# Optimization experiments

Hardware: AMD Instinct MI355X
Metric: run time of the kernel (lower is better)

## Reference

```python
import jax, jax.numpy as jnp
import numpy as np

B = 4194304  # batch
H = 32       # hidden width of TinyMLP


def _xavier(key, fan_in, fan_out, gain=0.5):
    lim = gain * np.sqrt(6.0 / (fan_in + fan_out))
    return jax.random.uniform(key, (fan_in, fan_out), jnp.float32, -lim, lim)


def setup_inputs() -> dict:
    key = jax.random.key(0)
    ks = jax.random.split(key, 7)
    return {
        "x1": jax.random.normal(ks[0], (B,), jnp.float32),
        "x2": jax.random.normal(ks[1], (B,), jnp.float32),
        "y1": jax.random.normal(ks[2], (B,), jnp.float32),
        "y2": jax.random.normal(ks[3], (B,), jnp.float32),
        "W1": _xavier(ks[4], 2, H),
        "b1": jnp.zeros((H,), jnp.float32),
        "W2": _xavier(ks[5], H, H),
        "b2": jnp.zeros((H,), jnp.float32),
        "W3": _xavier(ks[6], H, 1),
        "b3": jnp.zeros((1,), jnp.float32),
    }


def reference(x1, x2, y1, y2, W1, b1, W2, b2, W3, b3):
    # Y: [B, 2]
    Y = jnp.stack([y1, y2], axis=1)

    def F_sum(Yv):
        h1 = jax.nn.sigmoid(Yv @ W1 + b1)   # [B, H]
        h2 = jax.nn.sigmoid(h1 @ W2 + b2)   # [B, H]
        return jnp.sum(h2 @ W3 + b3)        # scalar sum of F values

    dF_dY = jax.grad(F_sum)(Y)              # [B, 2], analytic input-gradient

    x1_out = x1 + dF_dY[:, 0]
    x2_out = x2 + dF_dY[:, 1]
    # Stack the 4 output streams as columns: (x1', x2', y1, y2)
    return jnp.stack([x1_out, x2_out, y1, y2], axis=1)
```

## Files before the change

### kernel.cpp

```cpp
#include <hip/hip_runtime.h>


#define H 32
#define NLOG2E (-1.4426950408889634f)

typedef __attribute__((ext_vector_type(8))) short bf16x8;
typedef __attribute__((ext_vector_type(16))) float f32x16;
typedef __attribute__((ext_vector_type(2))) float f32x2;
typedef __attribute__((ext_vector_type(2))) __bf16 bfx2;

#define MFMA32 __builtin_amdgcn_mfma_f32_32x32x16_bf16

__device__ __forceinline__ int cvt_pk_bf16(float a, float b) {
    f32x2 f; f[0] = a; f[1] = b;
    bfx2 r = __builtin_convertvector(f, bfx2);
    return __builtin_bit_cast(int, r);
}
__device__ __forceinline__ float pklo(int p) {
    unsigned u = (unsigned)p << 16; return __builtin_bit_cast(float, u);
}
__device__ __forceinline__ float pkhi(int p) {
    unsigned u = (unsigned)p & 0xFFFF0000u; return __builtin_bit_cast(float, u);
}

__device__ __forceinline__ void plane32_swap(int &d, int &s) {
    asm volatile("v_permlane32_swap_b32 %0, %1" : "+v"(d), "+v"(s));
}

__global__ __launch_bounds__(256, 6) void tinymlp_mfma_kernel(
    const float* __restrict__ x1, const float* __restrict__ x2,
    const float* __restrict__ y1, const float* __restrict__ y2,
    const float* __restrict__ W1, const float* __restrict__ b1,
    const float* __restrict__ W2, const float* __restrict__ b2,
    const float* __restrict__ W3,
    float4* __restrict__ out, int ntiles)
{
    const int tid  = threadIdx.x;
    const int lane = tid & 63;
    const int n    = lane & 31;
    const int q5   = lane >> 5;

    union U4 { int i[4]; bf16x8 v; };
    U4 A_z1, A_z2a, A_z2b, A_dh1a, A_dh1b, A_dya, A_dyb;

    #pragma unroll
    for (int t = 0; t < 4; ++t) {
        const int j0 = 8 * q5 + 2 * t;
        const int j1 = j0 + 1;
        A_z2a.i[t] = cvt_pk_bf16(NLOG2E * W2[j0 * H + n],        NLOG2E * W2[j1 * H + n]);
        A_z2b.i[t] = cvt_pk_bf16(NLOG2E * W2[(16 + j0) * H + n], NLOG2E * W2[(16 + j1) * H + n]);
        A_dh1a.i[t] = cvt_pk_bf16(W2[n * H + j0] * W3[j0],           W2[n * H + j1] * W3[j1]);
        A_dh1b.i[t] = cvt_pk_bf16(W2[n * H + 16 + j0] * W3[16 + j0], W2[n * H + 16 + j1] * W3[16 + j1]);
        A_dya.i[t] = (n < 2) ? cvt_pk_bf16(W1[n * H + j0],      W1[n * H + j1])      : 0;
        A_dyb.i[t] = (n < 2) ? cvt_pk_bf16(W1[n * H + 16 + j0], W1[n * H + 16 + j1]) : 0;
    }

    A_z1.i[0] = A_z1.i[1] = A_z1.i[2] = A_z1.i[3] = 0;
    if (q5 == 0) {
        const float wa = NLOG2E * W1[n];
        const float wb = NLOG2E * W1[H + n];
        const float bv = NLOG2E * b1[n];
        const int hi  = cvt_pk_bf16(wa, wb);
        const int lo  = cvt_pk_bf16(wa - pklo(hi), wb - pkhi(hi));
        const int bh  = cvt_pk_bf16(bv, 0.f);
        const int bhl = cvt_pk_bf16(bv, bv - pklo(bh));
        A_z1.i[0] = hi; A_z1.i[1] = lo; A_z1.i[2] = hi; A_z1.i[3] = bhl;
    }

    f32x16 b2C;
    #pragma unroll
    for (int t = 0; t < 4; ++t) {
        const float4 bt = *(const float4*)&b2[8 * t + 4 * q5];
        b2C[4 * t + 0] = NLOG2E * bt.x; b2C[4 * t + 1] = NLOG2E * bt.y;
        b2C[4 * t + 2] = NLOG2E * bt.z; b2C[4 * t + 3] = NLOG2E * bt.w;
    }

    f32x16 zf16;
    #pragma unroll
    for (int r = 0; r < 16; ++r) zf16[r] = 0.f;

    const int gwave  = (blockIdx.x * blockDim.x + tid) >> 6;
    const int nwaves = (gridDim.x * blockDim.x) >> 6;
    unsigned idx = (unsigned)gwave * 32 + (unsigned)n;
    const unsigned step = (unsigned)nwaves * 32;

    for (int tt = gwave; tt < ntiles; tt += nwaves) {
        float y1v = 0.f, y2v = 0.f, xv1 = 0.f, xv2 = 0.f;
        if (lane < 32) {
            y1v = y1[idx]; y2v = y2[idx];
            xv1 = x1[idx]; xv2 = x2[idx];
        }

        U4 uY;
        const int pkHI = cvt_pk_bf16(y1v, y2v);
        const int pkLO = cvt_pk_bf16(y1v - pklo(pkHI), y2v - pkhi(pkHI));
        uY.i[0] = pkHI; uY.i[1] = pkHI; uY.i[2] = pkLO;
        uY.i[3] = 0x3F803F80;

        const f32x16 acc = MFMA32(A_z1.v, uY.v, zf16, 0, 0, 0);

        int P[8];
        #pragma unroll
        for (int h = 0; h < 2; ++h) {
            const int o = 8 * h;
            f32x2 A, Bv, Cv, Dv;
            A[0]  = __builtin_amdgcn_exp2f(acc[o + 0]);
            A[1]  = __builtin_amdgcn_exp2f(acc[o + 1]);
            Bv[0] = __builtin_amdgcn_exp2f(acc[o + 2]);
            Bv[1] = __builtin_amdgcn_exp2f(acc[o + 3]);
            Cv[0] = __builtin_amdgcn_exp2f(acc[o + 4]);
            Cv[1] = __builtin_amdgcn_exp2f(acc[o + 5]);
            Dv[0] = __builtin_amdgcn_exp2f(acc[o + 6]);
            Dv[1] = __builtin_amdgcn_exp2f(acc[o + 7]);
            A += 1.0f; Bv += 1.0f; Cv += 1.0f; Dv += 1.0f;
            const f32x2 M1 = A * Bv, M2 = Cv * Dv, M = M1 * M2;
            const float r = __builtin_amdgcn_rcpf(M[0] * M[1]);
            f32x2 R; R[0] = r * M[1]; R[1] = r * M[0];
            const f32x2 N1 = R * M2, N2 = R * M1;
            const f32x2 S0 = Bv * N1, S1 = A * N1, S2 = Dv * N2, S3 = Cv * N2;
            P[4 * h + 0] = cvt_pk_bf16(S0[0], S0[1]);
            P[4 * h + 1] = cvt_pk_bf16(S1[0], S1[1]);
            P[4 * h + 2] = cvt_pk_bf16(S2[0], S2[1]);
            P[4 * h + 3] = cvt_pk_bf16(S3[0], S3[1]);
        }

        U4 B1f, B2f;
        {
            int a0 = P[0], a2 = P[2]; plane32_swap(a0, a2);
            int a1 = P[1], a3 = P[3]; plane32_swap(a1, a3);
            B1f.i[0] = a0; B1f.i[1] = a1; B1f.i[2] = a2; B1f.i[3] = a3;
            int b0 = P[4], b2i = P[6]; plane32_swap(b0, b2i);
            int b1i = P[5], b3 = P[7]; plane32_swap(b1i, b3);
            B2f.i[0] = b0; B2f.i[1] = b1i; B2f.i[2] = b2i; B2f.i[3] = b3;
        }

        f32x16 zz = MFMA32(A_z2a.v, B1f.v, b2C, 0, 0, 0);
        zz = MFMA32(A_z2b.v, B2f.v, zz, 0, 0, 0);

        U4 D1f, D2f;
        #pragma unroll
        for (int h = 0; h < 2; ++h) {
            const int o = 8 * h;
            f32x2 A, Bv, Cv, Dv;
            A[0]  = __builtin_amdgcn_exp2f(zz[o + 0]);
            A[1]  = __builtin_amdgcn_exp2f(zz[o + 1]);
            Bv[0] = __builtin_amdgcn_exp2f(zz[o + 2]);
            Bv[1] = __builtin_amdgcn_exp2f(zz[o + 3]);
            Cv[0] = __builtin_amdgcn_exp2f(zz[o + 4]);
            Cv[1] = __builtin_amdgcn_exp2f(zz[o + 5]);
            Dv[0] = __builtin_amdgcn_exp2f(zz[o + 6]);
            Dv[1] = __builtin_amdgcn_exp2f(zz[o + 7]);
            A += 1.0f; Bv += 1.0f; Cv += 1.0f; Dv += 1.0f;
            const f32x2 M1 = A * Bv, M2 = Cv * Dv, M = M1 * M2;
            const float r = __builtin_amdgcn_rcpf(M[0] * M[1]);
            f32x2 R; R[0] = r * M[1]; R[1] = r * M[0];
            const f32x2 N1 = R * M2, N2 = R * M1;
            f32x2 S0 = Bv * N1, S1 = A * N1, S2 = Dv * N2, S3 = Cv * N2;
            S0 = __builtin_elementwise_fma(-S0, S0, S0);
            S1 = __builtin_elementwise_fma(-S1, S1, S1);
            S2 = __builtin_elementwise_fma(-S2, S2, S2);
            S3 = __builtin_elementwise_fma(-S3, S3, S3);
            U4& Df = h ? D2f : D1f;
            Df.i[0] = cvt_pk_bf16(S0[0], S0[1]);
            Df.i[1] = cvt_pk_bf16(S1[0], S1[1]);
            Df.i[2] = cvt_pk_bf16(S2[0], S2[1]);
            Df.i[3] = cvt_pk_bf16(S3[0], S3[1]);
        }
        plane32_swap(D1f.i[0], D1f.i[2]);
        plane32_swap(D1f.i[1], D1f.i[3]);
        plane32_swap(D2f.i[0], D2f.i[2]);
        plane32_swap(D2f.i[1], D2f.i[3]);

        f32x16 dh = MFMA32(A_dh1a.v, D1f.v, zf16, 0, 0, 0);
        dh = MFMA32(A_dh1b.v, D2f.v, dh, 0, 0, 0);

        U4 E1f, E2f;
        #pragma unroll
        for (int t = 0; t < 4; ++t) {
            U4& Ef = (t & 2) ? E2f : E1f;
            const int sl = 2 * (t & 1);
            f32x2 sv, gg;
            sv[0] = pklo(P[2 * t]); sv[1] = pkhi(P[2 * t]);
            sv = __builtin_elementwise_fma(-sv, sv, sv);
            gg[0] = dh[4 * t]; gg[1] = dh[4 * t + 1]; gg *= sv;
            Ef.i[sl] = cvt_pk_bf16(gg[0], gg[1]);
            sv[0] = pklo(P[2 * t + 1]); sv[1] = pkhi(P[2 * t + 1]);
            sv = __builtin_elementwise_fma(-sv, sv, sv);
            gg[0] = dh[4 * t + 2]; gg[1] = dh[4 * t + 3]; gg *= sv;
            Ef.i[sl + 1] = cvt_pk_bf16(gg[0], gg[1]);
        }
        plane32_swap(E1f.i[0], E1f.i[2]);
        plane32_swap(E1f.i[1], E1f.i[3]);
        plane32_swap(E2f.i[0], E2f.i[2]);
        plane32_swap(E2f.i[1], E2f.i[3]);

        f32x16 ay = MFMA32(A_dya.v, E1f.v, zf16, 0, 0, 0);
        ay = MFMA32(A_dyb.v, E2f.v, ay, 0, 0, 0);

        if (lane < 32) {
            float4 o;
            o.x = xv1 + ay[0];
            o.y = xv2 + ay[1];
            o.z = y1v;
            o.w = y2v;
            out[idx] = o;
        }

        idx += step;
    }
}

extern "C" void kernel_launch(void* const* d_in, const int* in_sizes, int n_in,
                              void* d_out, int out_size, void* d_ws, size_t ws_size,
                              hipStream_t stream) {
    const float* x1 = (const float*)d_in[0];
    const float* x2 = (const float*)d_in[1];
    const float* y1 = (const float*)d_in[2];
    const float* y2 = (const float*)d_in[3];
    const float* W1 = (const float*)d_in[4];
    const float* b1 = (const float*)d_in[5];
    const float* W2 = (const float*)d_in[6];
    const float* b2 = (const float*)d_in[7];
    const float* W3 = (const float*)d_in[8];

    const int n = in_sizes[0];
    const int ntiles = n / 32;
    const int block = 256;
    const int grid = 1536;
    tinymlp_mfma_kernel<<<grid, block, 0, stream>>>(
        x1, x2, y1, y2, W1, b1, W2, b2, W3, (float4*)d_out, ntiles);
}
```

Measured before the change: 208.6 us.

## Process two 32-row tiles per wave iteration to interleave MFMA chains

Each loop iteration now handles two independent tiles, A and B, with their MFMA and sigmoid stages interleaved. This is meant to hide MFMA latency and the serial dependency stalls within a single wave through instruction-level parallelism. To pay for the extra register use, the occupancy target in launch_bounds drops from 6 to 4 and the grid shrinks from 1536 to 1024 blocks. The code assumes ntiles is even, because odd leftover tiles would be dropped.

```diff
diff --git a/kernel.cpp b/kernel.cpp
--- a/kernel.cpp
+++ b/kernel.cpp
@@ -27,7 +27,7 @@
     asm volatile("v_permlane32_swap_b32 %0, %1" : "+v"(d), "+v"(s));
 }
 
-__global__ __launch_bounds__(256, 6) void tinymlp_mfma_kernel(
+__global__ __launch_bounds__(256, 4) void tinymlp_mfma_kernel(
     const float* __restrict__ x1, const float* __restrict__ x2,
     const float* __restrict__ y1, const float* __restrict__ y2,
     const float* __restrict__ W1, const float* __restrict__ b1,
@@ -79,39 +79,24 @@
     #pragma unroll
     for (int r = 0; r < 16; ++r) zf16[r] = 0.f;
 
-    const int gwave  = (blockIdx.x * blockDim.x + tid) >> 6;
-    const int nwaves = (gridDim.x * blockDim.x) >> 6;
-    unsigned idx = (unsigned)gwave * 32 + (unsigned)n;
-    const unsigned step = (unsigned)nwaves * 32;
-
-    for (int tt = gwave; tt < ntiles; tt += nwaves) {
-        float y1v = 0.f, y2v = 0.f, xv1 = 0.f, xv2 = 0.f;
-        if (lane < 32) {
-            y1v = y1[idx]; y2v = y2[idx];
-            xv1 = x1[idx]; xv2 = x2[idx];
-        }
-
-        U4 uY;
-        const int pkHI = cvt_pk_bf16(y1v, y2v);
-        const int pkLO = cvt_pk_bf16(y1v - pklo(pkHI), y2v - pkhi(pkHI));
-        uY.i[0] = pkHI; uY.i[1] = pkHI; uY.i[2] = pkLO;
-        uY.i[3] = 0x3F803F80;
-
-        const f32x16 acc = MFMA32(A_z1.v, uY.v, zf16, 0, 0, 0);
-
-        int P[8];
+    auto mkY = [&](float a, float b, U4& u) {
+        const int hi = cvt_pk_bf16(a, b);
+        const int lo = cvt_pk_bf16(a - pklo(hi), b - pkhi(hi));
+        u.i[0] = hi; u.i[1] = hi; u.i[2] = lo; u.i[3] = 0x3F803F80;
+    };
+    auto sig8 = [&](const f32x16& z, int* P) {
         #pragma unroll
         for (int h = 0; h < 2; ++h) {
             const int o = 8 * h;
             f32x2 A, Bv, Cv, Dv;
-            A[0]  = __builtin_amdgcn_exp2f(acc[o + 0]);
-            A[1]  = __builtin_amdgcn_exp2f(acc[o + 1]);
-            Bv[0] = __builtin_amdgcn_exp2f(acc[o + 2]);
-            Bv[1] = __builtin_amdgcn_exp2f(acc[o + 3]);
-            Cv[0] = __builtin_amdgcn_exp2f(acc[o + 4]);
-            Cv[1] = __builtin_amdgcn_exp2f(acc[o + 5]);
-            Dv[0] = __builtin_amdgcn_exp2f(acc[o + 6]);
-            Dv[1] = __builtin_amdgcn_exp2f(acc[o + 7]);
+            A[0]  = __builtin_amdgcn_exp2f(z[o + 0]);
+            A[1]  = __builtin_amdgcn_exp2f(z[o + 1]);
+            Bv[0] = __builtin_amdgcn_exp2f(z[o + 2]);
+            Bv[1] = __builtin_amdgcn_exp2f(z[o + 3]);
+            Cv[0] = __builtin_amdgcn_exp2f(z[o + 4]);
+            Cv[1] = __builtin_amdgcn_exp2f(z[o + 5]);
+            Dv[0] = __builtin_amdgcn_exp2f(z[o + 6]);
+            Dv[1] = __builtin_amdgcn_exp2f(z[o + 7]);
             A += 1.0f; Bv += 1.0f; Cv += 1.0f; Dv += 1.0f;
             const f32x2 M1 = A * Bv, M2 = Cv * Dv, M = M1 * M2;
             const float r = __builtin_amdgcn_rcpf(M[0] * M[1]);
@@ -123,21 +108,16 @@
             P[4 * h + 2] = cvt_pk_bf16(S2[0], S2[1]);
             P[4 * h + 3] = cvt_pk_bf16(S3[0], S3[1]);
         }
-
-        U4 B1f, B2f;
-        {
-            int a0 = P[0], a2 = P[2]; plane32_swap(a0, a2);
-            int a1 = P[1], a3 = P[3]; plane32_swap(a1, a3);
-            B1f.i[0] = a0; B1f.i[1] = a1; B1f.i[2] = a2; B1f.i[3] = a3;
-            int b0 = P[4], b2i = P[6]; plane32_swap(b0, b2i);
-            int b1i = P[5], b3 = P[7]; plane32_swap(b1i, b3);
-            B2f.i[0] = b0; B2f.i[1] = b1i; B2f.i[2] = b2i; B2f.i[3] = b3;
-        }
-
-        f32x16 zz = MFMA32(A_z2a.v, B1f.v, b2C, 0, 0, 0);
-        zz = MFMA32(A_z2b.v, B2f.v, zz, 0, 0, 0);
-
-        U4 D1f, D2f;
+    };
+    auto pivP = [&](const int* P, U4& F1, U4& F2) {
+        int a0 = P[0], a2 = P[2]; plane32_swap(a0, a2);
+        int a1 = P[1], a3 = P[3]; plane32_swap(a1, a3);
+        F1.i[0] = a0; F1.i[1] = a1; F1.i[2] = a2; F1.i[3] = a3;
+        int b0 = P[4], b2i = P[6]; plane32_swap(b0, b2i);
+        int b1i = P[5], b3 = P[7]; plane32_swap(b1i, b3);
+        F2.i[0] = b0; F2.i[1] = b1i; F2.i[2] = b2i; F2.i[3] = b3;
+    };
+    auto dz2f = [&](const f32x16& zz, U4& D1, U4& D2) {
         #pragma unroll
         for (int h = 0; h < 2; ++h) {
             const int o = 8 * h;
@@ -160,24 +140,21 @@
             S1 = __builtin_elementwise_fma(-S1, S1, S1);
             S2 = __builtin_elementwise_fma(-S2, S2, S2);
             S3 = __builtin_elementwise_fma(-S3, S3, S3);
-            U4& Df = h ? D2f : D1f;
+            U4& Df = h ? D2 : D1;
             Df.i[0] = cvt_pk_bf16(S0[0], S0[1]);
             Df.i[1] = cvt_pk_bf16(S1[0], S1[1]);
             Df.i[2] = cvt_pk_bf16(S2[0], S2[1]);
             Df.i[3] = cvt_pk_bf16(S3[0], S3[1]);
         }
-        plane32_swap(D1f.i[0], D1f.i[2]);
-        plane32_swap(D1f.i[1], D1f.i[3]);
-        plane32_swap(D2f.i[0], D2f.i[2]);
-        plane32_swap(D2f.i[1], D2f.i[3]);
-
-        f32x16 dh = MFMA32(A_dh1a.v, D1f.v, zf16, 0, 0, 0);
-        dh = MFMA32(A_dh1b.v, D2f.v, dh, 0, 0, 0);
-
-        U4 E1f, E2f;
+        plane32_swap(D1.i[0], D1.i[2]);
+        plane32_swap(D1.i[1], D1.i[3]);
+        plane32_swap(D2.i[0], D2.i[2]);
+        plane32_swap(D2.i[1], D2.i[3]);
+    };
+    auto dz1f = [&](const f32x16& dh, const int* P, U4& E1, U4& E2) {
         #pragma unroll
         for (int t = 0; t < 4; ++t) {
-            U4& Ef = (t & 2) ? E2f : E1f;
+            U4& Ef = (t & 2) ? E2 : E1;
             const int sl = 2 * (t & 1);
             f32x2 sv, gg;
             sv[0] = pklo(P[2 * t]); sv[1] = pkhi(P[2 * t]);
@@ -189,21 +166,78 @@
             gg[0] = dh[4 * t + 2]; gg[1] = dh[4 * t + 3]; gg *= sv;
             Ef.i[sl + 1] = cvt_pk_bf16(gg[0], gg[1]);
         }
-        plane32_swap(E1f.i[0], E1f.i[2]);
-        plane32_swap(E1f.i[1], E1f.i[3]);
-        plane32_swap(E2f.i[0], E2f.i[2]);
-        plane32_swap(E2f.i[1], E2f.i[3]);
-
-        f32x16 ay = MFMA32(A_dya.v, E1f.v, zf16, 0, 0, 0);
-        ay = MFMA32(A_dyb.v, E2f.v, ay, 0, 0, 0);
-
+        plane32_swap(E1.i[0], E1.i[2]);
+        plane32_swap(E1.i[1], E1.i[3]);
+        plane32_swap(E2.i[0], E2.i[2]);
+        plane32_swap(E2.i[1], E2.i[3]);
+    };
+
+    const int gpair  = (blockIdx.x * blockDim.x + tid) >> 6;
+    const int nwaves = (gridDim.x * blockDim.x) >> 6;
+    const int npairs = ntiles >> 1;
+    unsigned idx = (unsigned)gpair * 64 + (unsigned)n;
+    const unsigned step = (unsigned)nwaves * 64;
+
+    for (int pp = gpair; pp < npairs; pp += nwaves) {
+        float yA1 = 0.f, yA2 = 0.f, xA1 = 0.f, xA2 = 0.f;
+        float yB1 = 0.f, yB2 = 0.f, xB1 = 0.f, xB2 = 0.f;
         if (lane < 32) {
-            float4 o;
-            o.x = xv1 + ay[0];
-            o.y = xv2 + ay[1];
-            o.z = y1v;
-            o.w = y2v;
-            out[idx] = o;
+            yA1 = y1[idx];      yA2 = y2[idx];
+            yB1 = y1[idx + 32]; yB2 = y2[idx + 32];
+            xA1 = x1[idx];      xA2 = x2[idx];
+            xB1 = x1[idx + 32]; xB2 = x2[idx + 32];
+        }
+
+        U4 uYA, uYB;
+        mkY(yA1, yA2, uYA);
+        mkY(yB1, yB2, uYB);
+        const f32x16 accA = MFMA32(A_z1.v, uYA.v, zf16, 0, 0, 0);
+        const f32x16 accB = MFMA32(A_z1.v, uYB.v, zf16, 0, 0, 0);
+
+        int PA[8], PB[8];
+        sig8(accA, PA);
+        sig8(accB, PB);
+
+        U4 B1A, B2A, B1B, B2B;
+        pivP(PA, B1A, B2A);
+        pivP(PB, B1B, B2B);
+
+        f32x16 zzA = MFMA32(A_z2a.v, B1A.v, b2C, 0, 0, 0);
+        f32x16 zzB = MFMA32(A_z2a.v, B1B.v, b2C, 0, 0, 0);
+        zzA = MFMA32(A_z2b.v, B2A.v, zzA, 0, 0, 0);
+        zzB = MFMA32(A_z2b.v, B2B.v, zzB, 0, 0, 0);
+
+        U4 D1A, D2A, D1B, D2B;
+        dz2f(zzA, D1A, D2A);
+        dz2f(zzB, D1B, D2B);
+
+        f32x16 dhA = MFMA32(A_dh1a.v, D1A.v, zf16, 0, 0, 0);
+        f32x16 dhB = MFMA32(A_dh1a.v, D1B.v, zf16, 0, 0, 0);
+        dhA = MFMA32(A_dh1b.v, D2A.v, dhA, 0, 0, 0);
+        dhB = MFMA32(A_dh1b.v, D2B.v, dhB, 0, 0, 0);
+
+        U4 E1A, E2A, E1B, E2B;
+        dz1f(dhA, PA, E1A, E2A);
+        dz1f(dhB, PB, E1B, E2B);
+
+        f32x16 ayA = MFMA32(A_dya.v, E1A.v, zf16, 0, 0, 0);
+        f32x16 ayB = MFMA32(A_dya.v, E1B.v, zf16, 0, 0, 0);
+        ayA = MFMA32(A_dyb.v, E2A.v, ayA, 0, 0, 0);
+        ayB = MFMA32(A_dyb.v, E2B.v, ayB, 0, 0, 0);
+
+        if (lane < 32) {
+            float4 oA;
+            oA.x = xA1 + ayA[0];
+            oA.y = xA2 + ayA[1];
+            oA.z = yA1;
+            oA.w = yA2;
+            out[idx] = oA;
+            float4 oB;
+            oB.x = xB1 + ayB[0];
+            oB.y = xB2 + ayB[1];
+            oB.z = yB1;
+            oB.w = yB2;
+            out[idx + 32] = oB;
         }
 
         idx += step;
@@ -226,7 +260,7 @@
     const int n = in_sizes[0];
     const int ntiles = n / 32;
     const int block = 256;
-    const int grid = 1536;
+    const int grid = 1024;
     tinymlp_mfma_kernel<<<grid, block, 0, stream>>>(
         x1, x2, y1, y2, W1, b1, W2, b2, W3, (float4*)d_out, ntiles);
 }
```

New measurement: 190.4 us. 1.1x faster.
